# Performance work log

Hardware: AMD Instinct MI355X
Metric: run time of the kernel (lower is better)

Reference implementation:

```python
import jax, jax.numpy as jnp
import numpy as np

N, E, F_IN, HID, HEADS = 50000, 800000, 128, 64, 4


def setup_inputs() -> dict:
    key = jax.random.key(0)
    ks = jax.random.split(key, 10)
    def nrm(k, shape, scale=0.05):
        return jax.random.normal(k, shape, dtype=jnp.float32) * scale
    return {
        "x": jax.random.normal(ks[0], (N, F_IN), dtype=jnp.float32),
        "edge_index": jax.random.randint(ks[1], (2, E), 0, N),
        "W1": nrm(ks[2], (F_IN, HEADS * HID)),
        "att_src1": nrm(ks[3], (HEADS, HID)),
        "att_dst1": nrm(ks[4], (HEADS, HID)),
        "b1": jnp.zeros((HEADS * HID,), jnp.float32),
        "W2": nrm(ks[5], (HEADS * HID, HID)),
        "att_src2": nrm(ks[6], (1, HID)),
        "att_dst2": nrm(ks[7], (1, HID)),
        "b2": jnp.zeros((HID,), jnp.float32),
        "Wc": nrm(ks[8], (HID, 2)),
        "bc": jnp.zeros((2,), jnp.float32),
    }


def _segment_softmax(scores, seg, num_segments):
    # scores: [E, H]; softmax over all edges sharing the same dst node
    m = jax.ops.segment_max(scores, seg, num_segments=num_segments)
    m = jnp.where(jnp.isfinite(m), m, 0.0)  # nodes with no in-edges
    e = jnp.exp(scores - m[seg])
    s = jax.ops.segment_sum(e, seg, num_segments=num_segments)
    return e / (s[seg] + 1e-16)


def _gat_layer(x, src, dst, W, a_src, a_dst, b):
    # PyG GATConv (concat=True): h = xW -> [N,H,C]; alpha_ij = softmax_i(leaky_relu(a_s.h_j + a_d.h_i))
    n_nodes = x.shape[0]
    H, C = a_src.shape
    h = (x @ W).reshape(n_nodes, H, C)
    s_src = jnp.einsum('nhc,hc->nh', h, a_src)  # [N,H]
    s_dst = jnp.einsum('nhc,hc->nh', h, a_dst)  # [N,H]
    e = jax.nn.leaky_relu(s_src[src] + s_dst[dst], 0.2)  # [E,H]
    alpha = _segment_softmax(e, dst, n_nodes)            # [E,H]
    msg = h[src] * alpha[:, :, None]                     # [E,H,C] gather+weight
    out = jax.ops.segment_sum(msg, dst, num_segments=n_nodes)  # scatter-add
    return out.reshape(n_nodes, H * C) + b


def reference(x, edge_index, W1, att_src1, att_dst1, b1, W2, att_src2, att_dst2, b2, Wc, bc):
    n_nodes = x.shape[0]
    loops = jnp.arange(n_nodes)  # add_self_loops=True (PyG default)
    src = jnp.concatenate([edge_index[0], loops])
    dst = jnp.concatenate([edge_index[1], loops])
    # dropout layers are identity in eval mode
    h = _gat_layer(x, src, dst, W1, att_src1, att_dst1, b1)
    h = jax.nn.elu(h)
    h = _gat_layer(h, src, dst, W2, att_src2, att_dst2, b2)
    return h @ Wc + bc
```

## Files before the change

### kernel.cpp

```cpp
#include <hip/hip_runtime.h>
#include <hip/hip_fp16.h>
#include <math.h>

#define F_IN 128
#define C1 256
#define NH1 4
#define C2 64

typedef __attribute__((ext_vector_type(8))) _Float16 f16x8;
typedef __attribute__((ext_vector_type(4))) float f32x4;
typedef __attribute__((ext_vector_type(2))) float f32x2;

__device__ __forceinline__ float lrelu(float x) { return x >= 0.f ? x : 0.2f * x; }
__device__ __forceinline__ float elu(float x) { return x > 0.f ? x : expm1f(x); }
__device__ __forceinline__ int rli(int v, int j) { return __builtin_amdgcn_readlane(v, j); }

__device__ __forceinline__ void pkfma(f32x2& acc, f32x2 a, f32x2 b) {
    asm("v_pk_fma_f32 %0, %1, %2, %0" : "+v"(acc) : "v"(a), "v"(b));
}

struct __align__(8) H4 { __half2 a, b; };

__global__ __launch_bounds__(256) void k_init(const float* __restrict__ W1,
                                              const float* __restrict__ aS1,
                                              const float* __restrict__ aD1,
                                              float* __restrict__ atS,
                                              float* __restrict__ atD) {
    int t3 = blockIdx.x * 256 + threadIdx.x;
    if (t3 < 1024) {
        bool isD = t3 >= 512;
        int r = t3 & 511;
        int h = r >> 7, k = r & 127;
        const float* a = isD ? aD1 : aS1;
        float s = 0.f;
        for (int c = 0; c < 64; ++c) s += W1[(size_t)k * C1 + h * 64 + c] * a[h * 64 + c];
        (isD ? atD : atS)[h * 128 + k] = s;
    }
}

__global__ __launch_bounds__(256) void k_edges_prep(
    const int* __restrict__ esrc, const int* __restrict__ edst,
    int* __restrict__ cnt, int* __restrict__ elist, int E, int N,
    int countBlocks, int prepBlocks,
    const float* __restrict__ W1, const float* __restrict__ W2,
    __half* __restrict__ W1T, __half* __restrict__ W2T,
    const float* __restrict__ x, const float* __restrict__ atS,
    const float* __restrict__ atD, __half* __restrict__ xh,
    float* __restrict__ sS, float* __restrict__ sD) {
    int b = blockIdx.x;
    if (b < countBlocks) {
        int base = b * 2048 + threadIdx.x;
        int ET = E + N;
        int sv[8], dv[8], pv[8];
#pragma unroll
        for (int k = 0; k < 8; ++k) {
            int e = base + k * 256;
            int ss = 0, dd = -1;
            if (e < ET) {
                if (e < E) { ss = esrc[e]; dd = edst[e]; } else { ss = dd = e - E; }
            }
            sv[k] = ss; dv[k] = dd;
        }
#pragma unroll
        for (int k = 0; k < 8; ++k)
            pv[k] = (dv[k] >= 0) ? atomicAdd(&cnt[dv[k]], 1) : 0;
#pragma unroll
        for (int k = 0; k < 8; ++k)
            if (dv[k] >= 0 && pv[k] < 64) elist[(dv[k] << 6) + pv[k]] = sv[k];
    } else if (b < countBlocks + prepBlocks) {
        int tid = (b - countBlocks) * 256 + threadIdx.x;
        if (tid < F_IN * C1) {
            int k = tid >> 8, n = tid & 255;
            W1T[n * F_IN + k] = __float2half(W1[tid]);
        }
        int t2 = tid - F_IN * C1;
        if (t2 >= 0 && t2 < C1 * C2) {
            int k = t2 >> 6, n = t2 & 63;
            W2T[n * C1 + k] = __float2half(W2[t2]);
        }
    } else {
        int n = (b - countBlocks - prepBlocks) * 4 + (threadIdx.x >> 6);
        if (n >= N) return;
        int l = threadIdx.x & 63;
        float2 xv = *(const float2*)(x + (size_t)n * F_IN + l * 2);
        *(__half2*)(xh + (size_t)n * F_IN + l * 2) = __floats2half2_rn(xv.x, xv.y);
        float p[8];
#pragma unroll
        for (int h = 0; h < 4; ++h) {
            float2 a = *(const float2*)(atS + h * 128 + l * 2);
            float2 bb = *(const float2*)(atD + h * 128 + l * 2);
            p[h]     = xv.x * a.x + xv.y * a.y;
            p[4 + h] = xv.x * bb.x + xv.y * bb.y;
        }
#pragma unroll
        for (int off = 1; off < 64; off <<= 1) {
#pragma unroll
            for (int j = 0; j < 8; ++j) p[j] += __shfl_xor(p[j], off, 64);
        }
        if (l == 0) {
            *(float4*)(sS + n * 4) = make_float4(p[0], p[1], p[2], p[3]);
            *(float4*)(sD + n * 4) = make_float4(p[4], p[5], p[6], p[7]);
        }
    }
}

__global__ __launch_bounds__(256) void k_aggr1(const int* __restrict__ elist,
                                               const int* __restrict__ cnt,
                                               const float* __restrict__ sS,
                                               const float* __restrict__ sD,
                                               const __half* __restrict__ xh,
                                               __half* __restrict__ agg, int N) {
    __shared__ __align__(16) float wA[4][64][8];
    int wv = threadIdx.x >> 6, l = threadIdx.x & 63;
    int d = blockIdx.x * 4 + wv;
    if (d >= N) return;
    int len = cnt[d]; if (len > 64) len = 64;
    int base = d << 6;
    float4 sd4 = *(const float4*)(sD + d * 4);
    const __half* xb = xh + l * 2;
    f32x2 a0 = {0.f, 0.f}, a1 = {0.f, 0.f}, a2 = {0.f, 0.f}, a3 = {0.f, 0.f};
    float4 den = {0.f, 0.f, 0.f, 0.f};
    int sl = 0;
    float4 w = {0.f, 0.f, 0.f, 0.f};
    if (l < len) {
        sl = elist[base + l];
        float4 s4 = *(const float4*)(sS + sl * 4);
        w.x = __expf(lrelu(s4.x + sd4.x));
        w.y = __expf(lrelu(s4.y + sd4.y));
        w.z = __expf(lrelu(s4.z + sd4.z));
        w.w = __expf(lrelu(s4.w + sd4.w));
        den.x = w.x; den.y = w.y; den.z = w.z; den.w = w.w;
    }
    *(float4*)&wA[wv][l][0] = make_float4(w.x, w.x, w.y, w.y);
    *(float4*)&wA[wv][l][4] = make_float4(w.z, w.z, w.w, w.w);
    __builtin_amdgcn_wave_barrier();
    int jm = (len + 3) & ~3;
    for (int j = 0; j < jm; j += 4) {
#pragma unroll
        for (int u = 0; u < 4; ++u) {
            int s = rli(sl, j + u);
            f32x4 q0 = *(const f32x4*)&wA[wv][j + u][0];
            f32x4 q1 = *(const f32x4*)&wA[wv][j + u][4];
            float2 f = __half22float2(*(const __half2*)(xb + ((size_t)(unsigned)s << 7)));
            f32x2 fv = {f.x, f.y};
            pkfma(a0, fv, f32x2{q0[0], q0[1]});
            pkfma(a1, fv, f32x2{q0[2], q0[3]});
            pkfma(a2, fv, f32x2{q1[0], q1[1]});
            pkfma(a3, fv, f32x2{q1[2], q1[3]});
        }
    }
#pragma unroll
    for (int off = 1; off < 64; off <<= 1) {
        den.x += __shfl_xor(den.x, off, 64);
        den.y += __shfl_xor(den.y, off, 64);
        den.z += __shfl_xor(den.z, off, 64);
        den.w += __shfl_xor(den.w, off, 64);
    }
    float i0 = 1.f / (den.x + 1e-16f), i1 = 1.f / (den.y + 1e-16f);
    float i2 = 1.f / (den.z + 1e-16f), i3 = 1.f / (den.w + 1e-16f);
    __half2* ag = (__half2*)(agg + (size_t)d * 512);
    ag[0 * 64 + l] = __floats2half2_rn(a0[0] * i0, a0[1] * i0);
    ag[1 * 64 + l] = __floats2half2_rn(a1[0] * i1, a1[1] * i1);
    ag[2 * 64 + l] = __floats2half2_rn(a2[0] * i2, a2[1] * i2);
    ag[3 * 64 + l] = __floats2half2_rn(a3[0] * i3, a3[1] * i3);
}

__global__ __launch_bounds__(256) void k_gemm12(
    const __half* __restrict__ agg, const __half* __restrict__ W1T,
    const float* __restrict__ b1, const __half* __restrict__ W2T,
    const float* __restrict__ aS, const float* __restrict__ aD,
    __half* __restrict__ h2h, float* __restrict__ sS, float* __restrict__ sD, int N) {
    __shared__ __align__(16) char smem[65536];
    __half* As  = (__half*)smem;
    __half* Bs1 = (__half*)(smem + 16384);
    __half* Bs2 = (__half*)smem;
    __half* o1L = (__half*)(smem + 32768);
    int t = threadIdx.x;
    int rowBase = blockIdx.x * 64;
    int lane = t & 63, wv = t >> 6;
    int lm = lane & 15, lk = lane >> 4;
    int rA = wv * 16 + lm;
    int row = rowBase + rA;

    for (int h = 0; h < 4; ++h) {
        __syncthreads();
        {
            int r = t >> 2;
            const uint4* src = (const uint4*)(agg + (size_t)(rowBase + r) * 512 + h * 128);
#pragma unroll
            for (int j = 0; j < 4; ++j) {
                int g = (t & 3) * 4 + j;
                uint4 v = {0, 0, 0, 0};
                if (rowBase + r < N) v = src[g];
                *(uint4*)&As[r * 128 + (g ^ (r & 7)) * 8] = v;
            }
        }
        {
            int r = t >> 2;
            const uint4* src = (const uint4*)(W1T + (size_t)(h * 64 + r) * 128);
#pragma unroll
            for (int j = 0; j < 4; ++j) {
                int g = (t & 3) * 4 + j;
                *(uint4*)&Bs1[r * 128 + (g ^ (r & 7)) * 8] = src[g];
            }
        }
        __syncthreads();
        f32x4 acc[4];
#pragma unroll
        for (int nt = 0; nt < 4; ++nt) acc[nt] = f32x4{0.f, 0.f, 0.f, 0.f};
#pragma unroll
        for (int kt = 0; kt < 4; ++kt) {
            int gs = ((kt * 4 + lk) ^ (lm & 7)) * 8;
            f16x8 af = *(const f16x8*)&As[rA * 128 + gs];
#pragma unroll
            for (int nt = 0; nt < 4; ++nt) {
                f16x8 bf = *(const f16x8*)&Bs1[(nt * 16 + lm) * 128 + gs];
                acc[nt] = __builtin_amdgcn_mfma_f32_16x16x32_f16(bf, af, acc[nt], 0, 0, 0);
            }
        }
#pragma unroll
        for (int nt = 0; nt < 4; ++nt) {
            int c = h * 64 + nt * 16 + lk * 4;
            float4 bb = *(const float4*)(b1 + c);
            H4 hv;
            hv.a = __floats2half2_rn(elu(acc[nt][0] + bb.x), elu(acc[nt][1] + bb.y));
            hv.b = __floats2half2_rn(elu(acc[nt][2] + bb.z), elu(acc[nt][3] + bb.w));
            int g = c >> 3;
            int gs2 = (g & ~7) | ((g & 7) ^ (rA & 7));
            *(H4*)((char*)o1L + rA * 512 + gs2 * 16 + (c & 7) * 2) = hv;
        }
    }
    __syncthreads();
    {
        int n = t & 63, gb = (t >> 6) * 8;
        const uint4* src = (const uint4*)(W2T + (size_t)n * C1);
#pragma unroll
        for (int j = 0; j < 8; ++j) {
            int g = gb + j;
            int gs = (g & ~7) | ((g & 7) ^ (n & 7));
            *(uint4*)&Bs2[n * 256 + gs * 8] = src[g];
        }
    }
    __syncthreads();

    f32x4 acc2[4];
#pragma unroll
    for (int nt = 0; nt < 4; ++nt) acc2[nt] = f32x4{0.f, 0.f, 0.f, 0.f};
#pragma unroll
    for (int kt2 = 0; kt2 < 8; ++kt2) {
        int g = kt2 * 4 + lk;
        int gs = (g & ~7) | ((g & 7) ^ (lm & 7));
        f16x8 af = *(const f16x8*)&o1L[rA * 256 + gs * 8];
#pragma unroll
        for (int nt = 0; nt < 4; ++nt) {
            f16x8 bf = *(const f16x8*)&Bs2[(nt * 16 + lm) * 256 + gs * 8];
            acc2[nt] = __builtin_amdgcn_mfma_f32_16x16x32_f16(bf, af, acc2[nt], 0, 0, 0);
        }
    }
    float ps = 0.f, pd = 0.f;
#pragma unroll
    for (int nt = 0; nt < 4; ++nt) {
        int cbase = nt * 16 + lk * 4;
        float a0 = acc2[nt][0], a1 = acc2[nt][1], a2 = acc2[nt][2], a3 = acc2[nt][3];
        float4 s4 = *(const float4*)(aS + cbase);
        float4 d4 = *(const float4*)(aD + cbase);
        ps += a0 * s4.x + a1 * s4.y + a2 * s4.z + a3 * s4.w;
        pd += a0 * d4.x + a1 * d4.y + a2 * d4.z + a3 * d4.w;
        if (row < N) {
            H4 hv;
            hv.a = __floats2half2_rn(a0, a1);
            hv.b = __floats2half2_rn(a2, a3);
            *(H4*)(h2h + (size_t)row * C2 + cbase) = hv;
        }
    }
    ps += __shfl_xor(ps, 16, 64); ps += __shfl_xor(ps, 32, 64);
    pd += __shfl_xor(pd, 16, 64); pd += __shfl_xor(pd, 32, 64);
    if (lk == 0 && row < N) { sS[row] = ps; sD[row] = pd; }
}

__global__ __launch_bounds__(256) void k_aggr2(const int* __restrict__ elist,
                                               const int* __restrict__ cnt,
                                               const float* __restrict__ sS,
                                               const float* __restrict__ sD,
                                               const __half* __restrict__ h2h,
                                               const float* __restrict__ b2,
                                               const float* __restrict__ Wc,
                                               const float* __restrict__ bc,
                                               float* __restrict__ out, int N) {
    __shared__ int sw[4][64][4];
    int wv = threadIdx.x >> 6, l = threadIdx.x & 63;
    int d = blockIdx.x * 4 + wv;
    if (d >= N) return;
    int half = l >> 5, c2 = l & 31;
    float sdd = sD[d];
    int len = cnt[d]; if (len > 64) len = 64;
    int base = d << 6;
    f32x2 acc = {0.f, 0.f};
    float den = 0.f;
    const __half* hb = h2h + c2 * 2;
    int sl = 0; float w = 0.f;
    if (l < len) {
        sl = elist[base + l];
        w = __expf(lrelu(sS[sl] + sdd));
        den = w;
    }
    int4 e;
    e.x = sl; e.y = 0;
    e.z = __float_as_int(w); e.w = e.z;
    *(int4*)&sw[wv][l][0] = e;
    __builtin_amdgcn_wave_barrier();
    int pm = (len + 1) >> 1;
    int jm = (pm + 3) & ~3;
    for (int j = 0; j < jm; j += 4) {
        int4 q[4];
#pragma unroll
        for (int u = 0; u < 4; ++u)
            q[u] = *(const int4*)&sw[wv][2 * (j + u) + half][0];
        uint raw[4];
#pragma unroll
        for (int u = 0; u < 4; ++u)
            raw[u] = *(const uint*)(hb + ((size_t)(unsigned)q[u].x << 6));
#pragma unroll
        for (int u = 0; u < 4; ++u) {
            f32x2 wp = {__int_as_float(q[u].z), __int_as_float(q[u].w)};
            float2 f = __half22float2(*(__half2*)&raw[u]);
            pkfma(acc, f32x2{f.x, f.y}, wp);
        }
    }
#pragma unroll
    for (int off = 1; off < 64; off <<= 1) den += __shfl_xor(den, off, 64);
    float ax = acc[0], ay = acc[1];
    ax += __shfl_xor(ax, 32, 64);
    ay += __shfl_xor(ay, 32, 64);
    float inv = 1.f / (den + 1e-16f);
    float vx = ax * inv + b2[c2 * 2];
    float vy = ay * inv + b2[c2 * 2 + 1];
    float4 wc = *(const float4*)(Wc + c2 * 4);
    float p0 = vx * wc.x + vy * wc.z;
    float p1 = vx * wc.y + vy * wc.w;
    for (int off = 16; off; off >>= 1) {
        p0 += __shfl_down(p0, off, 32);
        p1 += __shfl_down(p1, off, 32);
    }
    if (l == 0) { out[d * 2 + 0] = p0 + bc[0]; out[d * 2 + 1] = p1 + bc[1]; }
}

extern "C" void kernel_launch(void* const* d_in, const int* in_sizes, int n_in,
                              void* d_out, int out_size, void* d_ws, size_t ws_size,
                              hipStream_t stream) {
    const float* x   = (const float*)d_in[0];
    const int*   ei  = (const int*)d_in[1];
    const float* W1  = (const float*)d_in[2];
    const float* aS1 = (const float*)d_in[3];
    const float* aD1 = (const float*)d_in[4];
    const float* b1  = (const float*)d_in[5];
    const float* W2  = (const float*)d_in[6];
    const float* aS2 = (const float*)d_in[7];
    const float* aD2 = (const float*)d_in[8];
    const float* b2  = (const float*)d_in[9];
    const float* Wc  = (const float*)d_in[10];
    const float* bc  = (const float*)d_in[11];
    float* out = (float*)d_out;

    int N = in_sizes[0] / F_IN;
    int E = in_sizes[1] / 2;
    const int* esrc = ei;
    const int* edst = ei + E;
    int ET = E + N;

    char* p = (char*)d_ws;
    __half* agg  = (__half*)p; p += (size_t)N * 512 * sizeof(__half);
    __half* xh   = (__half*)p; p += (size_t)N * F_IN * sizeof(__half);
    __half* h2h  = (__half*)p; p += (size_t)N * C2 * sizeof(__half);
    float* s1S   = (float*)p;  p += (size_t)N * NH1 * sizeof(float);
    float* s1D   = (float*)p;  p += (size_t)N * NH1 * sizeof(float);
    __half* W1T  = (__half*)p; p += (size_t)C1 * F_IN * sizeof(__half);
    __half* W2T  = (__half*)p; p += (size_t)C2 * C1 * sizeof(__half);
    float* atS   = (float*)p;  p += 512 * sizeof(float);
    float* atD   = (float*)p;  p += 512 * sizeof(float);
    float* s2S   = (float*)p;  p += (size_t)N * sizeof(float);
    float* s2D   = (float*)p;  p += (size_t)N * sizeof(float);
    int* cnt     = (int*)p;    p += (size_t)N * sizeof(int);
    int* elist   = (int*)p;    p += (size_t)N * 64 * sizeof(int);

    int countBlocks = (ET + 2047) / 2048;
    int prepBlocks  = (F_IN * C1 + C1 * C2) / 256;
    int xprepBlocks = (N + 3) / 4;

    hipMemsetAsync(cnt, 0, (size_t)N * 4, stream);
    k_init<<<4, 256, 0, stream>>>(W1, aS1, aD1, atS, atD);
    k_edges_prep<<<countBlocks + prepBlocks + xprepBlocks, 256, 0, stream>>>(
        esrc, edst, cnt, elist, E, N, countBlocks, prepBlocks,
        W1, W2, W1T, W2T, x, atS, atD, xh, s1S, s1D);

    k_aggr1<<<(N + 3) / 4, 256, 0, stream>>>(elist, cnt, s1S, s1D, xh, agg, N);
    k_gemm12<<<(N + 63) / 64, 256, 0, stream>>>(agg, W1T, b1, W2T, aS2, aD2, h2h, s2S, s2D, N);
    k_aggr2<<<(N + 3) / 4, 256, 0, stream>>>(elist, cnt, s2S, s2D, h2h, b2, Wc, bc, out, N);
}
```

Measured before the change: 183.6 us.

## Split edge bucketing by destination half to overlap with layer-1 aggregation

Edge bucketing is split into two passes by destination-node range. The second half's bucketing runs in the same launch as layer-1 aggregation of the first half, so the atomic-heavy scatter overlaps with gather work. Self-loops are no longer written to the edge list: counts start at 1 and slot 0 is implied to be the node itself, which removes the memset and the self-loop atomics. The cost is reading the edge arrays twice, plus one extra kernel launch.

```diff
diff --git a/kernel.cpp b/kernel.cpp
--- a/kernel.cpp
+++ b/kernel.cpp
@@ -21,99 +21,113 @@
 
 struct __align__(8) H4 { __half2 a, b; };
 
-__global__ __launch_bounds__(256) void k_init(const float* __restrict__ W1,
+__global__ __launch_bounds__(256) void k_init(int* __restrict__ cnt, int N, int zBlocks,
+                                              const float* __restrict__ W1,
                                               const float* __restrict__ aS1,
                                               const float* __restrict__ aD1,
                                               float* __restrict__ atS,
                                               float* __restrict__ atD) {
-    int t3 = blockIdx.x * 256 + threadIdx.x;
-    if (t3 < 1024) {
-        bool isD = t3 >= 512;
-        int r = t3 & 511;
-        int h = r >> 7, k = r & 127;
-        const float* a = isD ? aD1 : aS1;
-        float s = 0.f;
-        for (int c = 0; c < 64; ++c) s += W1[(size_t)k * C1 + h * 64 + c] * a[h * 64 + c];
-        (isD ? atD : atS)[h * 128 + k] = s;
-    }
-}
-
-__global__ __launch_bounds__(256) void k_edges_prep(
-    const int* __restrict__ esrc, const int* __restrict__ edst,
-    int* __restrict__ cnt, int* __restrict__ elist, int E, int N,
-    int countBlocks, int prepBlocks,
-    const float* __restrict__ W1, const float* __restrict__ W2,
-    __half* __restrict__ W1T, __half* __restrict__ W2T,
-    const float* __restrict__ x, const float* __restrict__ atS,
-    const float* __restrict__ atD, __half* __restrict__ xh,
-    float* __restrict__ sS, float* __restrict__ sD) {
-    int b = blockIdx.x;
-    if (b < countBlocks) {
-        int base = b * 2048 + threadIdx.x;
-        int ET = E + N;
-        int sv[8], dv[8], pv[8];
-#pragma unroll
-        for (int k = 0; k < 8; ++k) {
-            int e = base + k * 256;
-            int ss = 0, dd = -1;
-            if (e < ET) {
-                if (e < E) { ss = esrc[e]; dd = edst[e]; } else { ss = dd = e - E; }
-            }
-            sv[k] = ss; dv[k] = dd;
-        }
-#pragma unroll
-        for (int k = 0; k < 8; ++k)
-            pv[k] = (dv[k] >= 0) ? atomicAdd(&cnt[dv[k]], 1) : 0;
-#pragma unroll
-        for (int k = 0; k < 8; ++k)
-            if (dv[k] >= 0 && pv[k] < 64) elist[(dv[k] << 6) + pv[k]] = sv[k];
-    } else if (b < countBlocks + prepBlocks) {
-        int tid = (b - countBlocks) * 256 + threadIdx.x;
-        if (tid < F_IN * C1) {
-            int k = tid >> 8, n = tid & 255;
-            W1T[n * F_IN + k] = __float2half(W1[tid]);
-        }
-        int t2 = tid - F_IN * C1;
-        if (t2 >= 0 && t2 < C1 * C2) {
-            int k = t2 >> 6, n = t2 & 63;
-            W2T[n * C1 + k] = __float2half(W2[t2]);
-        }
+    if ((int)blockIdx.x < zBlocks) {
+        int i = blockIdx.x * 256 + threadIdx.x;
+        if (i < N) cnt[i] = 1;
     } else {
-        int n = (b - countBlocks - prepBlocks) * 4 + (threadIdx.x >> 6);
-        if (n >= N) return;
-        int l = threadIdx.x & 63;
-        float2 xv = *(const float2*)(x + (size_t)n * F_IN + l * 2);
-        *(__half2*)(xh + (size_t)n * F_IN + l * 2) = __floats2half2_rn(xv.x, xv.y);
-        float p[8];
-#pragma unroll
-        for (int h = 0; h < 4; ++h) {
-            float2 a = *(const float2*)(atS + h * 128 + l * 2);
-            float2 bb = *(const float2*)(atD + h * 128 + l * 2);
-            p[h]     = xv.x * a.x + xv.y * a.y;
-            p[4 + h] = xv.x * bb.x + xv.y * bb.y;
-        }
-#pragma unroll
-        for (int off = 1; off < 64; off <<= 1) {
-#pragma unroll
-            for (int j = 0; j < 8; ++j) p[j] += __shfl_xor(p[j], off, 64);
-        }
-        if (l == 0) {
-            *(float4*)(sS + n * 4) = make_float4(p[0], p[1], p[2], p[3]);
-            *(float4*)(sD + n * 4) = make_float4(p[4], p[5], p[6], p[7]);
-        }
-    }
-}
-
-__global__ __launch_bounds__(256) void k_aggr1(const int* __restrict__ elist,
-                                               const int* __restrict__ cnt,
-                                               const float* __restrict__ sS,
-                                               const float* __restrict__ sD,
-                                               const __half* __restrict__ xh,
-                                               __half* __restrict__ agg, int N) {
+        int t3 = (blockIdx.x - zBlocks) * 256 + threadIdx.x;
+        if (t3 < 1024) {
+            bool isD = t3 >= 512;
+            int r = t3 & 511;
+            int h = r >> 7, k = r & 127;
+            const float* a = isD ? aD1 : aS1;
+            float s = 0.f;
+            for (int c = 0; c < 64; ++c) s += W1[(size_t)k * C1 + h * 64 + c] * a[h * 64 + c];
+            (isD ? atD : atS)[h * 128 + k] = s;
+        }
+    }
+}
+
+__device__ __forceinline__ void dev_edges(int vb, int lo, int hi,
+                                          const int* __restrict__ esrc,
+                                          const int* __restrict__ edst,
+                                          int* __restrict__ cnt,
+                                          int* __restrict__ elist, int E) {
+    int base = vb * 2048 + threadIdx.x;
+    int sv[8], dv[8], pv[8];
+#pragma unroll
+    for (int k = 0; k < 8; ++k) {
+        int e = base + k * 256;
+        int ss = 0, dd = -1;
+        if (e < E) {
+            dd = edst[e];
+            ss = esrc[e];
+            if (dd < lo || dd >= hi) dd = -1;
+        }
+        sv[k] = ss; dv[k] = dd;
+    }
+#pragma unroll
+    for (int k = 0; k < 8; ++k)
+        pv[k] = (dv[k] >= 0) ? atomicAdd(&cnt[dv[k]], 1) : 64;
+#pragma unroll
+    for (int k = 0; k < 8; ++k)
+        if (dv[k] >= 0 && pv[k] < 64) elist[(dv[k] << 6) + pv[k]] = sv[k];
+}
+
+__device__ __forceinline__ void dev_wprep(int vb,
+                                          const float* __restrict__ W1,
+                                          const float* __restrict__ W2,
+                                          __half* __restrict__ W1T,
+                                          __half* __restrict__ W2T) {
+    int tid = vb * 256 + threadIdx.x;
+    if (tid < F_IN * C1) {
+        int k = tid >> 8, n = tid & 255;
+        W1T[n * F_IN + k] = __float2half(W1[tid]);
+    }
+    int t2 = tid - F_IN * C1;
+    if (t2 >= 0 && t2 < C1 * C2) {
+        int k = t2 >> 6, n = t2 & 63;
+        W2T[n * C1 + k] = __float2half(W2[t2]);
+    }
+}
+
+__device__ __forceinline__ void dev_xprep(int vb, const float* __restrict__ x,
+                                          const float* __restrict__ atS,
+                                          const float* __restrict__ atD,
+                                          __half* __restrict__ xh,
+                                          float* __restrict__ sS,
+                                          float* __restrict__ sD, int N) {
+    int n = vb * 4 + (threadIdx.x >> 6);
+    if (n >= N) return;
+    int l = threadIdx.x & 63;
+    float2 xv = *(const float2*)(x + (size_t)n * F_IN + l * 2);
+    *(__half2*)(xh + (size_t)n * F_IN + l * 2) = __floats2half2_rn(xv.x, xv.y);
+    float p[8];
+#pragma unroll
+    for (int h = 0; h < 4; ++h) {
+        float2 a = *(const float2*)(atS + h * 128 + l * 2);
+        float2 bb = *(const float2*)(atD + h * 128 + l * 2);
+        p[h]     = xv.x * a.x + xv.y * a.y;
+        p[4 + h] = xv.x * bb.x + xv.y * bb.y;
+    }
+#pragma unroll
+    for (int off = 1; off < 64; off <<= 1) {
+#pragma unroll
+        for (int j = 0; j < 8; ++j) p[j] += __shfl_xor(p[j], off, 64);
+    }
+    if (l == 0) {
+        *(float4*)(sS + n * 4) = make_float4(p[0], p[1], p[2], p[3]);
+        *(float4*)(sD + n * 4) = make_float4(p[4], p[5], p[6], p[7]);
+    }
+}
+
+__device__ __forceinline__ void dev_aggr1(int vb, int dLo, int dHi,
+                                          const int* __restrict__ elist,
+                                          const int* __restrict__ cnt,
+                                          const float* __restrict__ sS,
+                                          const float* __restrict__ sD,
+                                          const __half* __restrict__ xh,
+                                          __half* __restrict__ agg) {
     __shared__ __align__(16) float wA[4][64][8];
     int wv = threadIdx.x >> 6, l = threadIdx.x & 63;
-    int d = blockIdx.x * 4 + wv;
-    if (d >= N) return;
+    int d = dLo + vb * 4 + wv;
+    if (d >= dHi) return;
     int len = cnt[d]; if (len > 64) len = 64;
     int base = d << 6;
     float4 sd4 = *(const float4*)(sD + d * 4);
@@ -123,7 +137,7 @@
     int sl = 0;
     float4 w = {0.f, 0.f, 0.f, 0.f};
     if (l < len) {
-        sl = elist[base + l];
+        sl = (l == 0) ? d : elist[base + l];
         float4 s4 = *(const float4*)(sS + sl * 4);
         w.x = __expf(lrelu(s4.x + sd4.x));
         w.y = __expf(lrelu(s4.y + sd4.y));
@@ -163,6 +177,39 @@
     ag[1 * 64 + l] = __floats2half2_rn(a1[0] * i1, a1[1] * i1);
     ag[2 * 64 + l] = __floats2half2_rn(a2[0] * i2, a2[1] * i2);
     ag[3 * 64 + l] = __floats2half2_rn(a3[0] * i3, a3[1] * i3);
+}
+
+__global__ __launch_bounds__(256) void k_e_xprep(
+    const int* __restrict__ esrc, const int* __restrict__ edst,
+    int* __restrict__ cnt, int* __restrict__ elist, int E, int N, int Nh,
+    int eBlocks, int prepBlocks,
+    const float* __restrict__ W1, const float* __restrict__ W2,
+    __half* __restrict__ W1T, __half* __restrict__ W2T,
+    const float* __restrict__ x, const float* __restrict__ atS,
+    const float* __restrict__ atD, __half* __restrict__ xh,
+    float* __restrict__ sS, float* __restrict__ sD) {
+    int b = blockIdx.x;
+    if (b < eBlocks) dev_edges(b, 0, Nh, esrc, edst, cnt, elist, E);
+    else if (b < eBlocks + prepBlocks) dev_wprep(b - eBlocks, W1, W2, W1T, W2T);
+    else dev_xprep(b - eBlocks - prepBlocks, x, atS, atD, xh, sS, sD, N);
+}
+
+__global__ __launch_bounds__(256) void k_e_aggr1(
+    const int* __restrict__ esrc, const int* __restrict__ edst,
+    int* __restrict__ cnt, int* __restrict__ elist, int E, int N, int Nh,
+    int eBlocks,
+    const float* __restrict__ sS, const float* __restrict__ sD,
+    const __half* __restrict__ xh, __half* __restrict__ agg) {
+    int b = blockIdx.x;
+    if (b < eBlocks) dev_edges(b, Nh, N, esrc, edst, cnt, elist, E);
+    else dev_aggr1(b - eBlocks, 0, Nh, elist, cnt, sS, sD, xh, agg);
+}
+
+__global__ __launch_bounds__(256) void k_aggr1b(
+    const int* __restrict__ elist, const int* __restrict__ cnt,
+    const float* __restrict__ sS, const float* __restrict__ sD,
+    const __half* __restrict__ xh, __half* __restrict__ agg, int N, int Nh) {
+    dev_aggr1(blockIdx.x, Nh, N, elist, cnt, sS, sD, xh, agg);
 }
 
 __global__ __launch_bounds__(256) void k_gemm12(
@@ -300,7 +347,7 @@
     const __half* hb = h2h + c2 * 2;
     int sl = 0; float w = 0.f;
     if (l < len) {
-        sl = elist[base + l];
+        sl = (l == 0) ? d : elist[base + l];
         w = __expf(lrelu(sS[sl] + sdd));
         den = w;
     }
@@ -366,7 +413,6 @@
     int E = in_sizes[1] / 2;
     const int* esrc = ei;
     const int* edst = ei + E;
-    int ET = E + N;
 
     char* p = (char*)d_ws;
     __half* agg  = (__half*)p; p += (size_t)N * 512 * sizeof(__half);
@@ -383,17 +429,21 @@
     int* cnt     = (int*)p;    p += (size_t)N * sizeof(int);
     int* elist   = (int*)p;    p += (size_t)N * 64 * sizeof(int);
 
-    int countBlocks = (ET + 2047) / 2048;
+    int Nh = (((N / 2) + 3) / 4) * 4;
+    int zBlocks     = (N + 255) / 256;
+    int eBlocks     = (E + 2047) / 2048;
     int prepBlocks  = (F_IN * C1 + C1 * C2) / 256;
     int xprepBlocks = (N + 3) / 4;
-
-    hipMemsetAsync(cnt, 0, (size_t)N * 4, stream);
-    k_init<<<4, 256, 0, stream>>>(W1, aS1, aD1, atS, atD);
-    k_edges_prep<<<countBlocks + prepBlocks + xprepBlocks, 256, 0, stream>>>(
-        esrc, edst, cnt, elist, E, N, countBlocks, prepBlocks,
+    int a0Blocks    = (Nh + 3) / 4;
+    int a1Blocks    = (N - Nh + 3) / 4;
+
+    k_init<<<zBlocks + 4, 256, 0, stream>>>(cnt, N, zBlocks, W1, aS1, aD1, atS, atD);
+    k_e_xprep<<<eBlocks + prepBlocks + xprepBlocks, 256, 0, stream>>>(
+        esrc, edst, cnt, elist, E, N, Nh, eBlocks, prepBlocks,
         W1, W2, W1T, W2T, x, atS, atD, xh, s1S, s1D);
-
-    k_aggr1<<<(N + 3) / 4, 256, 0, stream>>>(elist, cnt, s1S, s1D, xh, agg, N);
+    k_e_aggr1<<<eBlocks + a0Blocks, 256, 0, stream>>>(
+        esrc, edst, cnt, elist, E, N, Nh, eBlocks, s1S, s1D, xh, agg);
+    k_aggr1b<<<a1Blocks, 256, 0, stream>>>(elist, cnt, s1S, s1D, xh, agg, N, Nh);
     k_gemm12<<<(N + 63) / 64, 256, 0, stream>>>(agg, W1T, b1, W2T, aS2, aD2, h2h, s2S, s2D, N);
     k_aggr2<<<(N + 3) / 4, 256, 0, stream>>>(elist, cnt, s2S, s2D, h2h, b2, Wc, bc, out, N);
 }
```

New measurement: 186.4 us. No clear change (+1.5%).

## Pad per-node counters, fold memset into init, implicit self-loop slot

Applied to the files above, without the earlier changes.

Per-node edge counters are padded to one per 64 bytes so that atomics on different destinations stop contending on the same cache line. The hipMemsetAsync is replaced by extra blocks in the init kernel that set each counter to 1, reserving slot 0 for the self loop. The aggregation kernels substitute the node id for slot 0 instead of reading it from the list, so the N self-loop edges no longer go through atomics. The cost is a counter array 16 times larger and strided, uncoalesced counter reads in the aggregation kernels.

```diff
diff --git a/kernel.cpp b/kernel.cpp
--- a/kernel.cpp
+++ b/kernel.cpp
@@ -6,6 +6,7 @@
 #define C1 256
 #define NH1 4
 #define C2 64
+#define CSH 4
 
 typedef __attribute__((ext_vector_type(8))) _Float16 f16x8;
 typedef __attribute__((ext_vector_type(4))) float f32x4;
@@ -21,20 +22,26 @@
 
 struct __align__(8) H4 { __half2 a, b; };
 
-__global__ __launch_bounds__(256) void k_init(const float* __restrict__ W1,
+__global__ __launch_bounds__(256) void k_init(int* __restrict__ cnt, int N, int zBlocks,
+                                              const float* __restrict__ W1,
                                               const float* __restrict__ aS1,
                                               const float* __restrict__ aD1,
                                               float* __restrict__ atS,
                                               float* __restrict__ atD) {
-    int t3 = blockIdx.x * 256 + threadIdx.x;
-    if (t3 < 1024) {
-        bool isD = t3 >= 512;
-        int r = t3 & 511;
-        int h = r >> 7, k = r & 127;
-        const float* a = isD ? aD1 : aS1;
-        float s = 0.f;
-        for (int c = 0; c < 64; ++c) s += W1[(size_t)k * C1 + h * 64 + c] * a[h * 64 + c];
-        (isD ? atD : atS)[h * 128 + k] = s;
+    if ((int)blockIdx.x < zBlocks) {
+        int i = blockIdx.x * 256 + threadIdx.x;
+        if (i < N) cnt[(size_t)i << CSH] = 1;
+    } else {
+        int t3 = (blockIdx.x - zBlocks) * 256 + threadIdx.x;
+        if (t3 < 1024) {
+            bool isD = t3 >= 512;
+            int r = t3 & 511;
+            int h = r >> 7, k = r & 127;
+            const float* a = isD ? aD1 : aS1;
+            float s = 0.f;
+            for (int c = 0; c < 64; ++c) s += W1[(size_t)k * C1 + h * 64 + c] * a[h * 64 + c];
+            (isD ? atD : atS)[h * 128 + k] = s;
+        }
     }
 }
 
@@ -50,20 +57,17 @@
     int b = blockIdx.x;
     if (b < countBlocks) {
         int base = b * 2048 + threadIdx.x;
-        int ET = E + N;
         int sv[8], dv[8], pv[8];
 #pragma unroll
         for (int k = 0; k < 8; ++k) {
             int e = base + k * 256;
             int ss = 0, dd = -1;
-            if (e < ET) {
-                if (e < E) { ss = esrc[e]; dd = edst[e]; } else { ss = dd = e - E; }
-            }
+            if (e < E) { ss = esrc[e]; dd = edst[e]; }
             sv[k] = ss; dv[k] = dd;
         }
 #pragma unroll
         for (int k = 0; k < 8; ++k)
-            pv[k] = (dv[k] >= 0) ? atomicAdd(&cnt[dv[k]], 1) : 0;
+            pv[k] = (dv[k] >= 0) ? atomicAdd(&cnt[(size_t)dv[k] << CSH], 1) : 64;
 #pragma unroll
         for (int k = 0; k < 8; ++k)
             if (dv[k] >= 0 && pv[k] < 64) elist[(dv[k] << 6) + pv[k]] = sv[k];
@@ -114,7 +118,7 @@
     int wv = threadIdx.x >> 6, l = threadIdx.x & 63;
     int d = blockIdx.x * 4 + wv;
     if (d >= N) return;
-    int len = cnt[d]; if (len > 64) len = 64;
+    int len = cnt[(size_t)d << CSH]; if (len > 64) len = 64;
     int base = d << 6;
     float4 sd4 = *(const float4*)(sD + d * 4);
     const __half* xb = xh + l * 2;
@@ -123,7 +127,7 @@
     int sl = 0;
     float4 w = {0.f, 0.f, 0.f, 0.f};
     if (l < len) {
-        sl = elist[base + l];
+        sl = (l == 0) ? d : elist[base + l];
         float4 s4 = *(const float4*)(sS + sl * 4);
         w.x = __expf(lrelu(s4.x + sd4.x));
         w.y = __expf(lrelu(s4.y + sd4.y));
@@ -293,14 +297,14 @@
     if (d >= N) return;
     int half = l >> 5, c2 = l & 31;
     float sdd = sD[d];
-    int len = cnt[d]; if (len > 64) len = 64;
+    int len = cnt[(size_t)d << CSH]; if (len > 64) len = 64;
     int base = d << 6;
     f32x2 acc = {0.f, 0.f};
     float den = 0.f;
     const __half* hb = h2h + c2 * 2;
     int sl = 0; float w = 0.f;
     if (l < len) {
-        sl = elist[base + l];
+        sl = (l == 0) ? d : elist[base + l];
         w = __expf(lrelu(sS[sl] + sdd));
         den = w;
     }
@@ -366,7 +370,6 @@
     int E = in_sizes[1] / 2;
     const int* esrc = ei;
     const int* edst = ei + E;
-    int ET = E + N;
 
     char* p = (char*)d_ws;
     __half* agg  = (__half*)p; p += (size_t)N * 512 * sizeof(__half);
@@ -380,15 +383,15 @@
     float* atD   = (float*)p;  p += 512 * sizeof(float);
     float* s2S   = (float*)p;  p += (size_t)N * sizeof(float);
     float* s2D   = (float*)p;  p += (size_t)N * sizeof(float);
-    int* cnt     = (int*)p;    p += (size_t)N * sizeof(int);
+    int* cnt     = (int*)p;    p += ((size_t)N << CSH) * sizeof(int);
     int* elist   = (int*)p;    p += (size_t)N * 64 * sizeof(int);
 
-    int countBlocks = (ET + 2047) / 2048;
+    int zBlocks     = (N + 255) / 256;
+    int countBlocks = (E + 2047) / 2048;
     int prepBlocks  = (F_IN * C1 + C1 * C2) / 256;
     int xprepBlocks = (N + 3) / 4;
 
-    hipMemsetAsync(cnt, 0, (size_t)N * 4, stream);
-    k_init<<<4, 256, 0, stream>>>(W1, aS1, aD1, atS, atD);
+    k_init<<<zBlocks + 4, 256, 0, stream>>>(cnt, N, zBlocks, W1, aS1, aD1, atS, atD);
     k_edges_prep<<<countBlocks + prepBlocks + xprepBlocks, 256, 0, stream>>>(
         esrc, edst, cnt, elist, E, N, countBlocks, prepBlocks,
         W1, W2, W1T, W2T, x, atS, atD, xh, s1S, s1D);
```

After: 171.9 us. -6.4%, faster.
